# Kernel optimization log

Hardware: AMD Instinct MI355X
Metric: run time of the kernel (lower is better)

Reference implementation:

```python
import jax, jax.numpy as jnp
import numpy as np

EPS = 1e-6

def _elu_feature_map(x):
    # fast_transformers default feature map: elu(x) + 1 (always positive)
    return jax.nn.elu(x) + 1.0

def setup_inputs() -> dict:
    key = jax.random.key(0)
    ks = jax.random.split(key, 7)
    f, n, c, hid = 1024, 64, 256, 1024
    s = 1.0 / np.sqrt(c)
    return {
        "x": jax.random.normal(ks[0], (f, n, c), dtype=jnp.float32),
        "Wq": jax.random.normal(ks[1], (c, hid), dtype=jnp.float32) * s,
        "bq": jax.random.normal(ks[2], (hid,), dtype=jnp.float32) * 0.01,
        "Wk": jax.random.normal(ks[3], (c, hid), dtype=jnp.float32) * s,
        "bk": jax.random.normal(ks[4], (hid,), dtype=jnp.float32) * 0.01,
        "Wv": jax.random.normal(ks[5], (c, hid), dtype=jnp.float32) * s,
        "bv": jax.random.normal(ks[6], (hid,), dtype=jnp.float32) * 0.01,
    }

def reference(x, Wq, bq, Wk, bk, Wv, bv):
    heads = 8
    f, n, c = x.shape
    xt = jnp.transpose(x, (1, 0, 2))  # (n, f, c): joints as batch, frames as sequence
    q = xt @ Wq + bq  # (n, f, hid)
    k = xt @ Wk + bk
    v = xt @ Wv + bv
    hid = q.shape[-1]
    d = hid // heads
    q = q.reshape(n, f, heads, d)
    k = k.reshape(n, f, heads, d)
    v = v.reshape(n, f, heads, d)
    # Linear (kernelized) attention, non-causal (FullMask + full LengthMask)
    Q = _elu_feature_map(q)  # (n, f, h, d)
    K = _elu_feature_map(k)
    KV = jnp.einsum('nshd,nshm->nhmd', K, v)          # (n, h, d_v, d_k)
    Ksum = K.sum(axis=1)                               # (n, h, d_k)
    Z = 1.0 / (jnp.einsum('nlhd,nhd->nlh', Q, Ksum) + EPS)  # (n, f, h)
    out = jnp.einsum('nlhd,nhmd,nlh->nlhm', Q, KV, Z)  # (n, f, h, d_v)
    # faithful to rearrange('f n h c -> n f (h c)') applied to (n, f, h, d):
    # swaps first two axes -> output shape (f, n, h*d)
    out = jnp.transpose(out, (1, 0, 2, 3)).reshape(f, n, hid)
    return out
```

## Files before the change

### kernel.cpp

```cpp
#include <hip/hip_runtime.h>
#include <hip/hip_bf16.h>

#define F 1024
#define N 64
#define C 256
#define HID 1024
#define NH 8
#define D 128

using bf16x8 = __attribute__((ext_vector_type(8))) short;
using u16x8  = __attribute__((ext_vector_type(8))) unsigned short;
using u16x4  = __attribute__((ext_vector_type(4))) unsigned short;
using f32x4  = __attribute__((ext_vector_type(4))) float;

__device__ __forceinline__ unsigned short f2b(float f) {
    union { float f; unsigned u; } v; v.f = f;
    unsigned u = v.u;
    unsigned r = (u + 0x7fffu + ((u >> 16) & 1u)) >> 16;
    return (unsigned short)r;
}
__device__ __forceinline__ float b2f(unsigned short h) {
    union { unsigned u; float f; } v; v.u = ((unsigned)h) << 16;
    return v.f;
}

__device__ __forceinline__ void load_lds16(const unsigned short* g, unsigned short* l) {
    __builtin_amdgcn_global_load_lds(
        (const __attribute__((address_space(1))) void*)g,
        (__attribute__((address_space(3))) void*)l, 16, 0, 0);
}

__global__ void k_conv_x(const float* __restrict__ x, unsigned short* __restrict__ xt) {
    int row = blockIdx.x * 4 + (threadIdx.x >> 6);
    int lane = threadIdx.x & 63;
    int fi = row >> 6, ni = row & 63;
    float4 a = *(const float4*)(x + row * C + lane * 4);
    u16x4 o;
    o[0] = f2b(a.x); o[1] = f2b(a.y); o[2] = f2b(a.z); o[3] = f2b(a.w);
    *(u16x4*)(xt + (ni * F + fi) * C + lane * 4) = o;
}

__global__ void k_conv_w(const float* __restrict__ Wq, const float* __restrict__ Wk,
                         const float* __restrict__ Wv, unsigned short* __restrict__ Wt) {
    int w = blockIdx.z;
    const float* W = (w == 0) ? Wq : ((w == 1) ? Wk : Wv);
    unsigned short* O = Wt + w * (HID * C);
    int n0 = blockIdx.x * 64, k0 = blockIdx.y * 64;
    __shared__ float t[64][65];
    int tx = threadIdx.x & 63, ty = threadIdx.x >> 6;
#pragma unroll
    for (int i = 0; i < 16; i++) {
        int kl = ty + i * 4;
        t[kl][tx] = W[(k0 + kl) * HID + n0 + tx];
    }
    __syncthreads();
#pragma unroll
    for (int i = 0; i < 16; i++) {
        int nl = ty + i * 4;
        O[(n0 + nl) * C + k0 + tx] = f2b(t[tx][nl]);
    }
}

__global__ __launch_bounds__(256, 2) void k_kv_fused(
    const unsigned short* __restrict__ xt, const unsigned short* __restrict__ Wt,
    const float* __restrict__ bk, const float* __restrict__ bv,
    unsigned short* __restrict__ KV, float* __restrict__ Ksum) {
    __shared__ unsigned short Ks[128 * 128];
    __shared__ unsigned short Vs[128 * 128];
    __shared__ unsigned short Sx[128 * 32];
    __shared__ unsigned short Sw[128 * 32];

    const int ni = blockIdx.x & 63, h = blockIdx.x >> 6;
    const int b = ni * NH + h;
    const int tid = threadIdx.x, lane = tid & 63, w = tid >> 6;
    const int quad = lane >> 4, l15 = lane & 15;
    const int wm = w >> 1, wn = w & 1;
    const int srow = lane >> 2, scol = (lane & 3) * 8;

    const unsigned short* xb  = xt + ni * (F * C);
    const unsigned short* Wkp = Wt + (HID * C) + (h * D) * C;
    const unsigned short* Wvp = Wt + 2 * (HID * C) + (h * D) * C;
    const float* bkp = bk + h * D;
    const float* bvp = bv + h * D;

    f32x4 acc2[4][4];
#pragma unroll
    for (int i = 0; i < 4; i++)
#pragma unroll
        for (int j = 0; j < 4; j++) acc2[i][j] = (f32x4)0.f;
    float ksacc = 0.f;
    const int zd = tid >> 1, zh = tid & 1;

#pragma unroll 1
    for (int ft = 0; ft < 8; ft++) {
        const unsigned short* xrow = xb + (ft * 128) * C;
#pragma unroll 1
        for (int pv = 0; pv < 2; pv++) {
            const unsigned short* Wp = pv ? Wvp : Wkp;
            f32x4 acc[4][4];
#pragma unroll
            for (int i = 0; i < 4; i++)
#pragma unroll
                for (int j = 0; j < 4; j++) acc[i][j] = (f32x4)0.f;
#pragma unroll
            for (int ks = 0; ks < 8; ks++) {
                const int kof = ks * 32;
                const unsigned short* ga = xrow + (w * 32 + srow) * C + kof + scol;
                const unsigned short* gw = Wp + (w * 32 + srow) * C + kof + scol;
                load_lds16(ga,          Sx + (w * 32) * 32);
                load_lds16(ga + 16 * C, Sx + (w * 32 + 16) * 32);
                load_lds16(gw,          Sw + (w * 32) * 32);
                load_lds16(gw + 16 * C, Sw + (w * 32 + 16) * 32);
                __syncthreads();
                bf16x8 af[4], bfr[4];
#pragma unroll
                for (int mb = 0; mb < 4; mb++)
                    af[mb] = *(const bf16x8*)(Sw + (wm * 64 + mb * 16 + l15) * 32 + quad * 8);
#pragma unroll
                for (int nb = 0; nb < 4; nb++)
                    bfr[nb] = *(const bf16x8*)(Sx + (wn * 64 + nb * 16 + l15) * 32 + quad * 8);
#pragma unroll
                for (int mb = 0; mb < 4; mb++)
#pragma unroll
                    for (int nb = 0; nb < 4; nb++)
                        acc[mb][nb] = __builtin_amdgcn_mfma_f32_16x16x32_bf16(
                            af[mb], bfr[nb], acc[mb][nb], 0, 0, 0);
                __syncthreads();
            }
            const float* bias = pv ? bvp : bkp;
            unsigned short* T = pv ? Vs : Ks;
#pragma unroll
            for (int mb = 0; mb < 4; mb++)
#pragma unroll
                for (int r = 0; r < 4; r++) {
                    int dd = wm * 64 + mb * 16 + quad * 4 + r;
                    float bb = bias[dd];
                    char* rowp = (char*)T + dd * 256;
                    int sw = (dd & 7) << 4;
#pragma unroll
                    for (int nb = 0; nb < 4; nb++) {
                        int fi = wn * 64 + nb * 16 + l15;
                        float v = acc[mb][nb][r] + bb;
                        if (!pv) v = (v > 0.f) ? (v + 1.f) : __expf(v);
                        *(unsigned short*)(rowp + ((fi * 2) ^ sw)) = f2b(v);
                    }
                }
        }
        __syncthreads();
#pragma unroll
        for (int k0 = 0; k0 < 128; k0 += 32) {
            bf16x8 af[4], bfr[4];
#pragma unroll
            for (int mb = 0; mb < 4; mb++) {
                int m = wm * 64 + mb * 16 + l15;
                af[mb] = *(const bf16x8*)((const char*)Vs + m * 256 +
                                          (((k0 + quad * 8) * 2) ^ ((m & 7) << 4)));
            }
#pragma unroll
            for (int nb = 0; nb < 4; nb++) {
                int d = wn * 64 + nb * 16 + l15;
                bfr[nb] = *(const bf16x8*)((const char*)Ks + d * 256 +
                                           (((k0 + quad * 8) * 2) ^ ((d & 7) << 4)));
            }
#pragma unroll
            for (int mb = 0; mb < 4; mb++)
#pragma unroll
                for (int nb = 0; nb < 4; nb++)
                    acc2[mb][nb] = __builtin_amdgcn_mfma_f32_16x16x32_bf16(
                        af[mb], bfr[nb], acc2[mb][nb], 0, 0, 0);
        }
        {
            const char* kr = (const char*)Ks + zd * 256;
            int sw = (zd & 7) << 4;
#pragma unroll
            for (int c = 0; c < 8; c++) {
                u16x8 v = *(const u16x8*)(kr + (((zh * 8 + c) * 16) ^ sw));
#pragma unroll
                for (int j = 0; j < 8; j++) ksacc += b2f(v[j]);
            }
        }
    }

    unsigned short* KVp = KV + b * (D * D);
#pragma unroll
    for (int mb = 0; mb < 4; mb++)
#pragma unroll
        for (int r = 0; r < 4; r++) {
            int m = wm * 64 + mb * 16 + quad * 4 + r;
#pragma unroll
            for (int nb = 0; nb < 4; nb++) {
                int d = wn * 64 + nb * 16 + l15;
                KVp[m * D + d] = f2b(acc2[mb][nb][r]);
            }
        }
    __syncthreads();
    float* sred = (float*)Sx;
    sred[tid] = ksacc;
    __syncthreads();
    if (tid < 128) Ksum[b * D + tid] = sred[2 * tid] + sred[2 * tid + 1];
}

__global__ __launch_bounds__(256, 3) void k_out_fused(
    const unsigned short* __restrict__ xt, const unsigned short* __restrict__ Wt,
    const float* __restrict__ bq, const unsigned short* __restrict__ KV,
    const float* __restrict__ Ksum, float* __restrict__ out) {
    __shared__ unsigned short Qs[128 * 128];
    __shared__ unsigned short Sx[128 * 32];
    __shared__ unsigned short Sw[128 * 32];
    __shared__ float Kss[128];
    __shared__ float Zs[128];

    const int ni = blockIdx.x & 63, h = blockIdx.x >> 6;
    const int b = ni * NH + h;
    const int l0 = blockIdx.y * 128;
    const int tid = threadIdx.x, lane = tid & 63, w = tid >> 6;
    const int quad = lane >> 4, l15 = lane & 15;
    const int wm = w >> 1, wn = w & 1;
    const int srow = lane >> 2, scol = (lane & 3) * 8;

    if (tid < 128) Kss[tid] = Ksum[b * D + tid];

    const unsigned short* xrow = xt + (ni * F + l0) * C;
    const unsigned short* Wqp = Wt + (h * D) * C;

    f32x4 acc[4][4];
#pragma unroll
    for (int i = 0; i < 4; i++)
#pragma unroll
        for (int j = 0; j < 4; j++) acc[i][j] = (f32x4)0.f;
#pragma unroll
    for (int ks = 0; ks < 8; ks++) {
        const int kof = ks * 32;
        const unsigned short* ga = xrow + (w * 32 + srow) * C + kof + scol;
        const unsigned short* gw = Wqp + (w * 32 + srow) * C + kof + scol;
        load_lds16(ga,          Sx + (w * 32) * 32);
        load_lds16(ga + 16 * C, Sx + (w * 32 + 16) * 32);
        load_lds16(gw,          Sw + (w * 32) * 32);
        load_lds16(gw + 16 * C, Sw + (w * 32 + 16) * 32);
        __syncthreads();
        bf16x8 af[4], bfr[4];
#pragma unroll
        for (int mb = 0; mb < 4; mb++)
            af[mb] = *(const bf16x8*)(Sx + (wm * 64 + mb * 16 + l15) * 32 + quad * 8);
#pragma unroll
        for (int nb = 0; nb < 4; nb++)
            bfr[nb] = *(const bf16x8*)(Sw + (wn * 64 + nb * 16 + l15) * 32 + quad * 8);
#pragma unroll
        for (int mb = 0; mb < 4; mb++)
#pragma unroll
            for (int nb = 0; nb < 4; nb++)
                acc[mb][nb] = __builtin_amdgcn_mfma_f32_16x16x32_bf16(
                    af[mb], bfr[nb], acc[mb][nb], 0, 0, 0);
        __syncthreads();
    }
    {
        float bcol[4];
#pragma unroll
        for (int nb = 0; nb < 4; nb++) bcol[nb] = bq[h * D + wn * 64 + nb * 16 + l15];
#pragma unroll
        for (int mb = 0; mb < 4; mb++)
#pragma unroll
            for (int r = 0; r < 4; r++) {
                int fi = wm * 64 + mb * 16 + quad * 4 + r;
                char* rowp = (char*)Qs + fi * 256;
                int sw = (fi & 7) << 4;
#pragma unroll
                for (int nb = 0; nb < 4; nb++) {
                    int dd = wn * 64 + nb * 16 + l15;
                    float v = acc[mb][nb][r] + bcol[nb];
                    v = (v > 0.f) ? (v + 1.f) : __expf(v);
                    *(unsigned short*)(rowp + ((dd * 2) ^ sw)) = f2b(v);
                }
            }
    }
    __syncthreads();
    if (tid < 128) {
        const char* qr = (const char*)Qs + tid * 256;
        int sw = (tid & 7) << 4;
        float s = 0.f;
#pragma unroll
        for (int c = 0; c < 16; c++) {
            u16x8 v = *(const u16x8*)(qr + ((c * 16) ^ sw));
#pragma unroll
            for (int j = 0; j < 8; j++) s += b2f(v[j]) * Kss[c * 8 + j];
        }
        Zs[tid] = 1.f / (s + 1e-6f);
    }
    __syncthreads();
    const unsigned short* KVp = KV + b * (D * D);
    f32x4 o4[4][4];
#pragma unroll
    for (int i = 0; i < 4; i++)
#pragma unroll
        for (int j = 0; j < 4; j++) o4[i][j] = (f32x4)0.f;
#pragma unroll
    for (int k0 = 0; k0 < 128; k0 += 32) {
        bf16x8 af[4], bfr[4];
#pragma unroll
        for (int mb = 0; mb < 4; mb++) {
            int m = wm * 64 + mb * 16 + l15;
            af[mb] = *(const bf16x8*)(KVp + m * D + k0 + quad * 8);
        }
#pragma unroll
        for (int nb = 0; nb < 4; nb++) {
            int l = wn * 64 + nb * 16 + l15;
            bfr[nb] = *(const bf16x8*)((const char*)Qs + l * 256 +
                                       (((k0 + quad * 8) * 2) ^ ((l & 7) << 4)));
        }
#pragma unroll
        for (int mb = 0; mb < 4; mb++)
#pragma unroll
            for (int nb = 0; nb < 4; nb++)
                o4[mb][nb] = __builtin_amdgcn_mfma_f32_16x16x32_bf16(
                    af[mb], bfr[nb], o4[mb][nb], 0, 0, 0);
    }
#pragma unroll
    for (int nb = 0; nb < 4; nb++) {
        int l = wn * 64 + nb * 16 + l15;
        float z = Zs[l];
        float* op = out + ((l0 + l) * N + ni) * HID + h * D;
#pragma unroll
        for (int mb = 0; mb < 4; mb++) {
            int m0 = wm * 64 + mb * 16 + quad * 4;
            float4 vv;
            vv.x = o4[mb][nb][0] * z;
            vv.y = o4[mb][nb][1] * z;
            vv.z = o4[mb][nb][2] * z;
            vv.w = o4[mb][nb][3] * z;
            *(float4*)(op + m0) = vv;
        }
    }
}

extern "C" void kernel_launch(void* const* d_in, const int* in_sizes, int n_in,
                              void* d_out, int out_size, void* d_ws, size_t ws_size,
                              hipStream_t stream) {
    const float* x  = (const float*)d_in[0];
    const float* Wq = (const float*)d_in[1];
    const float* bq = (const float*)d_in[2];
    const float* Wk = (const float*)d_in[3];
    const float* bk = (const float*)d_in[4];
    const float* Wv = (const float*)d_in[5];
    const float* bv = (const float*)d_in[6];
    float* out = (float*)d_out;
    char* ws = (char*)d_ws;

    unsigned short* xt   = (unsigned short*)(ws);
    unsigned short* Wt   = (unsigned short*)(ws + 33554432);
    unsigned short* KVb  = (unsigned short*)(ws + 35127296);
    float*          Ksum = (float*)(ws + 51904512);

    k_conv_x<<<16384, 256, 0, stream>>>(x, xt);
    k_conv_w<<<dim3(16, 4, 3), 256, 0, stream>>>(Wq, Wk, Wv, Wt);
    k_kv_fused<<<512, 256, 0, stream>>>(xt, Wt, bk, bv, KVb, Ksum);
    k_out_fused<<<dim3(512, 8), 256, 0, stream>>>(xt, Wt, bq, KVb, Ksum, out);
}
```

Baseline: 609.3 us.

## Split KV reduction over frame tiles across blocks with fp32 atomics

```diff
diff --git a/kernel.cpp b/kernel.cpp
--- a/kernel.cpp
+++ b/kernel.cpp
@@ -28,6 +28,12 @@
     __builtin_amdgcn_global_load_lds(
         (const __attribute__((address_space(1))) void*)g,
         (__attribute__((address_space(3))) void*)l, 16, 0, 0);
+}
+
+__global__ void k_zero(float* __restrict__ p) {
+    int i = (blockIdx.x * 256 + threadIdx.x) * 4;
+    float4 z; z.x = 0.f; z.y = 0.f; z.z = 0.f; z.w = 0.f;
+    *(float4*)(p + i) = z;
 }
 
 __global__ void k_conv_x(const float* __restrict__ x, unsigned short* __restrict__ xt) {
@@ -64,140 +70,148 @@
 __global__ __launch_bounds__(256, 2) void k_kv_fused(
     const unsigned short* __restrict__ xt, const unsigned short* __restrict__ Wt,
     const float* __restrict__ bk, const float* __restrict__ bv,
-    unsigned short* __restrict__ KV, float* __restrict__ Ksum) {
+    float* __restrict__ KV32, float* __restrict__ Ksum) {
     __shared__ unsigned short Ks[128 * 128];
     __shared__ unsigned short Vs[128 * 128];
     __shared__ unsigned short Sx[128 * 32];
     __shared__ unsigned short Sw[128 * 32];
 
     const int ni = blockIdx.x & 63, h = blockIdx.x >> 6;
+    const int ft = blockIdx.y;
     const int b = ni * NH + h;
     const int tid = threadIdx.x, lane = tid & 63, w = tid >> 6;
     const int quad = lane >> 4, l15 = lane & 15;
     const int wm = w >> 1, wn = w & 1;
     const int srow = lane >> 2, scol = (lane & 3) * 8;
 
-    const unsigned short* xb  = xt + ni * (F * C);
+    const unsigned short* xrow = xt + (ni * F + ft * 128) * C;
     const unsigned short* Wkp = Wt + (HID * C) + (h * D) * C;
     const unsigned short* Wvp = Wt + 2 * (HID * C) + (h * D) * C;
     const float* bkp = bk + h * D;
     const float* bvp = bv + h * D;
 
+#pragma unroll 1
+    for (int pv = 0; pv < 2; pv++) {
+        const unsigned short* Wp = pv ? Wvp : Wkp;
+        f32x4 acc[4][4];
+#pragma unroll
+        for (int i = 0; i < 4; i++)
+#pragma unroll
+            for (int j = 0; j < 4; j++) acc[i][j] = (f32x4)0.f;
+#pragma unroll
+        for (int ks = 0; ks < 8; ks++) {
+            const int kof = ks * 32;
+            const unsigned short* ga = xrow + (w * 32 + srow) * C + kof + scol;
+            const unsigned short* gw = Wp + (w * 32 + srow) * C + kof + scol;
+            load_lds16(ga,          Sx + (w * 32) * 32);
+            load_lds16(ga + 16 * C, Sx + (w * 32 + 16) * 32);
+            load_lds16(gw,          Sw + (w * 32) * 32);
+            load_lds16(gw + 16 * C, Sw + (w * 32 + 16) * 32);
+            __syncthreads();
+            bf16x8 af[4], bfr[4];
+#pragma unroll
+            for (int mb = 0; mb < 4; mb++)
+                af[mb] = *(const bf16x8*)(Sw + (wm * 64 + mb * 16 + l15) * 32 + quad * 8);
+#pragma unroll
+            for (int nb = 0; nb < 4; nb++)
+                bfr[nb] = *(const bf16x8*)(Sx + (wn * 64 + nb * 16 + l15) * 32 + quad * 8);
+#pragma unroll
+            for (int mb = 0; mb < 4; mb++)
+#pragma unroll
+                for (int nb = 0; nb < 4; nb++)
+                    acc[mb][nb] = __builtin_amdgcn_mfma_f32_16x16x32_bf16(
+                        af[mb], bfr[nb], acc[mb][nb], 0, 0, 0);
+            __syncthreads();
+        }
+        const float* bias = pv ? bvp : bkp;
+        unsigned short* T = pv ? Vs : Ks;
+#pragma unroll
+        for (int mb = 0; mb < 4; mb++)
+#pragma unroll
+            for (int r = 0; r < 4; r++) {
+                int dd = wm * 64 + mb * 16 + quad * 4 + r;
+                float bb = bias[dd];
+                char* rowp = (char*)T + dd * 256;
+                int sw = (dd & 7) << 4;
+#pragma unroll
+                for (int nb = 0; nb < 4; nb++) {
+                    int fi = wn * 64 + nb * 16 + l15;
+                    float v = acc[mb][nb][r] + bb;
+                    if (!pv) v = (v > 0.f) ? (v + 1.f) : __expf(v);
+                    *(unsigned short*)(rowp + ((fi * 2) ^ sw)) = f2b(v);
+                }
+            }
+        __syncthreads();
+    }
+
     f32x4 acc2[4][4];
 #pragma unroll
     for (int i = 0; i < 4; i++)
 #pragma unroll
         for (int j = 0; j < 4; j++) acc2[i][j] = (f32x4)0.f;
+#pragma unroll
+    for (int k0 = 0; k0 < 128; k0 += 32) {
+        bf16x8 af[4], bfr[4];
+#pragma unroll
+        for (int mb = 0; mb < 4; mb++) {
+            int m = wm * 64 + mb * 16 + l15;
+            af[mb] = *(const bf16x8*)((const char*)Vs + m * 256 +
+                                      (((k0 + quad * 8) * 2) ^ ((m & 7) << 4)));
+        }
+#pragma unroll
+        for (int nb = 0; nb < 4; nb++) {
+            int d = wn * 64 + nb * 16 + l15;
+            bfr[nb] = *(const bf16x8*)((const char*)Ks + d * 256 +
+                                       (((k0 + quad * 8) * 2) ^ ((d & 7) << 4)));
+        }
+#pragma unroll
+        for (int mb = 0; mb < 4; mb++)
+#pragma unroll
+            for (int nb = 0; nb < 4; nb++)
+                acc2[mb][nb] = __builtin_amdgcn_mfma_f32_16x16x32_bf16(
+                    af[mb], bfr[nb], acc2[mb][nb], 0, 0, 0);
+    }
+
     float ksacc = 0.f;
-    const int zd = tid >> 1, zh = tid & 1;
-
-#pragma unroll 1
-    for (int ft = 0; ft < 8; ft++) {
-        const unsigned short* xrow = xb + (ft * 128) * C;
-#pragma unroll 1
-        for (int pv = 0; pv < 2; pv++) {
-            const unsigned short* Wp = pv ? Wvp : Wkp;
-            f32x4 acc[4][4];
-#pragma unroll
-            for (int i = 0; i < 4; i++)
-#pragma unroll
-                for (int j = 0; j < 4; j++) acc[i][j] = (f32x4)0.f;
-#pragma unroll
-            for (int ks = 0; ks < 8; ks++) {
-                const int kof = ks * 32;
-                const unsigned short* ga = xrow + (w * 32 + srow) * C + kof + scol;
-                const unsigned short* gw = Wp + (w * 32 + srow) * C + kof + scol;
-                load_lds16(ga,          Sx + (w * 32) * 32);
-                load_lds16(ga + 16 * C, Sx + (w * 32 + 16) * 32);
-                load_lds16(gw,          Sw + (w * 32) * 32);
-                load_lds16(gw + 16 * C, Sw + (w * 32 + 16) * 32);
-                __syncthreads();
-                bf16x8 af[4], bfr[4];
-#pragma unroll
-                for (int mb = 0; mb < 4; mb++)
-                    af[mb] = *(const bf16x8*)(Sw + (wm * 64 + mb * 16 + l15) * 32 + quad * 8);
-#pragma unroll
-                for (int nb = 0; nb < 4; nb++)
-                    bfr[nb] = *(const bf16x8*)(Sx + (wn * 64 + nb * 16 + l15) * 32 + quad * 8);
-#pragma unroll
-                for (int mb = 0; mb < 4; mb++)
-#pragma unroll
-                    for (int nb = 0; nb < 4; nb++)
-                        acc[mb][nb] = __builtin_amdgcn_mfma_f32_16x16x32_bf16(
-                            af[mb], bfr[nb], acc[mb][nb], 0, 0, 0);
-                __syncthreads();
-            }
-            const float* bias = pv ? bvp : bkp;
-            unsigned short* T = pv ? Vs : Ks;
-#pragma unroll
-            for (int mb = 0; mb < 4; mb++)
-#pragma unroll
-                for (int r = 0; r < 4; r++) {
-                    int dd = wm * 64 + mb * 16 + quad * 4 + r;
-                    float bb = bias[dd];
-                    char* rowp = (char*)T + dd * 256;
-                    int sw = (dd & 7) << 4;
-#pragma unroll
-                    for (int nb = 0; nb < 4; nb++) {
-                        int fi = wn * 64 + nb * 16 + l15;
-                        float v = acc[mb][nb][r] + bb;
-                        if (!pv) v = (v > 0.f) ? (v + 1.f) : __expf(v);
-                        *(unsigned short*)(rowp + ((fi * 2) ^ sw)) = f2b(v);
-                    }
-                }
-        }
-        __syncthreads();
-#pragma unroll
-        for (int k0 = 0; k0 < 128; k0 += 32) {
-            bf16x8 af[4], bfr[4];
-#pragma unroll
-            for (int mb = 0; mb < 4; mb++) {
-                int m = wm * 64 + mb * 16 + l15;
-                af[mb] = *(const bf16x8*)((const char*)Vs + m * 256 +
-                                          (((k0 + quad * 8) * 2) ^ ((m & 7) << 4)));
-            }
+    {
+        const int zd = tid >> 1, zh = tid & 1;
+        const char* kr = (const char*)Ks + zd * 256;
+        int sw = (zd & 7) << 4;
+#pragma unroll
+        for (int c = 0; c < 8; c++) {
+            u16x8 v = *(const u16x8*)(kr + (((zh * 8 + c) * 16) ^ sw));
+#pragma unroll
+            for (int j = 0; j < 8; j++) ksacc += b2f(v[j]);
+        }
+    }
+    __syncthreads();
+    float* sred = (float*)Sx;
+    sred[tid] = ksacc;
+    __syncthreads();
+    if (tid < 128) atomicAdd(&Ksum[b * D + tid], sred[2 * tid] + sred[2 * tid + 1]);
+
+    float* KVp = KV32 + b * (D * D);
+#pragma unroll
+    for (int mb = 0; mb < 4; mb++)
+#pragma unroll
+        for (int r = 0; r < 4; r++) {
+            int m = wm * 64 + mb * 16 + quad * 4 + r;
 #pragma unroll
             for (int nb = 0; nb < 4; nb++) {
                 int d = wn * 64 + nb * 16 + l15;
-                bfr[nb] = *(const bf16x8*)((const char*)Ks + d * 256 +
-                                           (((k0 + quad * 8) * 2) ^ ((d & 7) << 4)));
+                atomicAdd(KVp + m * D + d, acc2[mb][nb][r]);
             }
-#pragma unroll
-            for (int mb = 0; mb < 4; mb++)
-#pragma unroll
-                for (int nb = 0; nb < 4; nb++)
-                    acc2[mb][nb] = __builtin_amdgcn_mfma_f32_16x16x32_bf16(
-                        af[mb], bfr[nb], acc2[mb][nb], 0, 0, 0);
-        }
-        {
-            const char* kr = (const char*)Ks + zd * 256;
-            int sw = (zd & 7) << 4;
-#pragma unroll
-            for (int c = 0; c < 8; c++) {
-                u16x8 v = *(const u16x8*)(kr + (((zh * 8 + c) * 16) ^ sw));
-#pragma unroll
-                for (int j = 0; j < 8; j++) ksacc += b2f(v[j]);
-            }
-        }
-    }
-
-    unsigned short* KVp = KV + b * (D * D);
-#pragma unroll
-    for (int mb = 0; mb < 4; mb++)
-#pragma unroll
-        for (int r = 0; r < 4; r++) {
-            int m = wm * 64 + mb * 16 + quad * 4 + r;
-#pragma unroll
-            for (int nb = 0; nb < 4; nb++) {
-                int d = wn * 64 + nb * 16 + l15;
-                KVp[m * D + d] = f2b(acc2[mb][nb][r]);
-            }
-        }
-    __syncthreads();
-    float* sred = (float*)Sx;
-    sred[tid] = ksacc;
-    __syncthreads();
-    if (tid < 128) Ksum[b * D + tid] = sred[2 * tid] + sred[2 * tid + 1];
+        }
+}
+
+__global__ void k_conv_kv(const float* __restrict__ KV32, unsigned short* __restrict__ KVb) {
+    int i = (blockIdx.x * 256 + threadIdx.x) * 8;
+    float4 a = *(const float4*)(KV32 + i);
+    float4 c = *(const float4*)(KV32 + i + 4);
+    u16x8 o;
+    o[0] = f2b(a.x); o[1] = f2b(a.y); o[2] = f2b(a.z); o[3] = f2b(a.w);
+    o[4] = f2b(c.x); o[5] = f2b(c.y); o[6] = f2b(c.z); o[7] = f2b(c.w);
+    *(u16x8*)(KVb + i) = o;
 }
 
 __global__ __launch_bounds__(256, 3) void k_out_fused(
@@ -348,10 +362,14 @@
     unsigned short* xt   = (unsigned short*)(ws);
     unsigned short* Wt   = (unsigned short*)(ws + 33554432);
     unsigned short* KVb  = (unsigned short*)(ws + 35127296);
-    float*          Ksum = (float*)(ws + 51904512);
+    float*          KV32 = (float*)(ws + 51904512);
+    float*          Ksum = (float*)(ws + 85458944);
+
+    k_zero<<<8256, 256, 0, stream>>>(KV32);
 
     k_conv_x<<<16384, 256, 0, stream>>>(x, xt);
     k_conv_w<<<dim3(16, 4, 3), 256, 0, stream>>>(Wq, Wk, Wv, Wt);
-    k_kv_fused<<<512, 256, 0, stream>>>(xt, Wt, bk, bv, KVb, Ksum);
+    k_kv_fused<<<dim3(512, 8), 256, 0, stream>>>(xt, Wt, bk, bv, KV32, Ksum);
+    k_conv_kv<<<4096, 256, 0, stream>>>(KV32, KVb);
     k_out_fused<<<dim3(512, 8), 256, 0, stream>>>(xt, Wt, bq, KVb, Ksum, out);
 }
```

Measured after the change: 671.2 us. 1.1x slower.
